# Kernel optimization log

Measured on AMD Instinct MI355X. Metric: run time of the kernel, lower is better.

Reference implementation:

```python
import jax, jax.numpy as jnp
import numpy as np

N, E = 50000, 800000
NFEAT, NHID, HEADS, NCLASS = 256, 16, 8, 40


def _gat_conv(x, src, dst, W, att_src, att_dst, bias, heads, out_ch, concat, num_nodes):
    # x: [N, F_in]; W: [F_in, heads*out_ch]; att_*: [heads, out_ch]; bias matches output dim
    h = (x @ W).reshape(num_nodes, heads, out_ch)          # [N, H, C]
    a_src = jnp.einsum('nhc,hc->nh', h, att_src)           # [N, H]
    a_dst = jnp.einsum('nhc,hc->nh', h, att_dst)           # [N, H]
    logits = jax.nn.leaky_relu(a_src[src] + a_dst[dst], negative_slope=0.2)  # [E, H]
    # segment softmax over incoming edges of each destination node
    m = jax.ops.segment_max(logits, dst, num_segments=num_nodes)
    e = jnp.exp(logits - m[dst])
    denom = jax.ops.segment_sum(e, dst, num_segments=num_nodes)
    alpha = e / (denom[dst] + 1e-16)                       # [E, H]
    msg = h[src] * alpha[:, :, None]                       # [E, H, C]
    out = jax.ops.segment_sum(msg, dst, num_segments=num_nodes)  # [N, H, C]
    out = out.reshape(num_nodes, heads * out_ch) if concat else out.mean(axis=1)
    return out + bias


def setup_inputs() -> dict:
    key = jax.random.key(0)
    ks = jax.random.split(key, 10)
    x = jax.random.normal(ks[0], (N, NFEAT), dtype=jnp.float32)
    edge_index = jax.random.randint(ks[1], (2, E), 0, N, dtype=jnp.int64)
    s = 0.1
    W1 = jax.random.normal(ks[2], (NFEAT, HEADS * NHID), dtype=jnp.float32) * s
    att_src1 = jax.random.normal(ks[3], (HEADS, NHID), dtype=jnp.float32) * s
    att_dst1 = jax.random.normal(ks[4], (HEADS, NHID), dtype=jnp.float32) * s
    b1 = jnp.zeros((HEADS * NHID,), dtype=jnp.float32)
    W2 = jax.random.normal(ks[5], (HEADS * NHID, NCLASS), dtype=jnp.float32) * s
    att_src2 = jax.random.normal(ks[6], (1, NCLASS), dtype=jnp.float32) * s
    att_dst2 = jax.random.normal(ks[7], (1, NCLASS), dtype=jnp.float32) * s
    b2 = jnp.zeros((NCLASS,), dtype=jnp.float32)
    return dict(x=x, edge_index=edge_index, W1=W1, att_src1=att_src1, att_dst1=att_dst1,
                b1=b1, W2=W2, att_src2=att_src2, att_dst2=att_dst2, b2=b2)


def reference(x, edge_index, W1, att_src1, att_dst1, b1, W2, att_src2, att_dst2, b2):
    # add self-loops (PyG GATConv default)
    loops = jnp.arange(N, dtype=edge_index.dtype)
    src = jnp.concatenate([edge_index[0], loops])
    dst = jnp.concatenate([edge_index[1], loops])
    # dropout layers are identity in eval mode
    h = _gat_conv(x, src, dst, W1, att_src1, att_dst1, b1, HEADS, NHID, True, N)
    h = jax.nn.elu(h)
    out = _gat_conv(h, src, dst, W2, att_src2, att_dst2, b2, 1, NCLASS, False, N)
    return jax.nn.log_softmax(out, axis=1)
```

## Files before the change

kernel.cpp:

```cpp
#include <hip/hip_runtime.h>
#include <math.h>

#define NODES 50000
#define NEDGE 800000
#define ETOT  (NEDGE + NODES)
#define NF    256
#define F1    128
#define NHEAD 8
#define NHID  16
#define NC    40
#define ELLCAP 64
#define SG_BLOCKS 4103
#define SG_GEMMCUT 3910

typedef __attribute__((ext_vector_type(8))) short bf16x8;
typedef __attribute__((ext_vector_type(4))) float f32x4;
typedef __attribute__((ext_vector_type(2))) float f32x2;

__device__ __forceinline__ float bflo(unsigned u) { return __uint_as_float(u << 16); }
__device__ __forceinline__ float bfhi(unsigned u) { return __uint_as_float(u & 0xffff0000u); }
__device__ __forceinline__ unsigned short f2bf(float f) {
    unsigned u = __float_as_uint(f);
    unsigned r = u + 0x7fffu + ((u >> 16) & 1u);
    return (unsigned short)(r >> 16);
}
__device__ __forceinline__ unsigned pk2(float a, float b) {
    return (unsigned)f2bf(a) | ((unsigned)f2bf(b) << 16);
}

__global__ void detect_k(const unsigned* __restrict__ u, unsigned* __restrict__ flag) {
    int t = threadIdx.x;
    if (u[2 * t + 1] != 0u) atomicOr(flag, 1u);
}

__global__ void prepW12(const float* __restrict__ W1, const float* __restrict__ atts1,
                        const float* __restrict__ attd1,
                        const float* __restrict__ W2, const float* __restrict__ atts2,
                        const float* __restrict__ attd2,
                        unsigned short* __restrict__ W1t, unsigned short* __restrict__ W2e) {
    int b = blockIdx.x;
    int k = threadIdx.x;
    if (b < 144) {
        int n = b;
        float v;
        if (n < 128) {
            v = W1[(size_t)k * F1 + n];
        } else if (n < 136) {
            int h = n - 128; v = 0.f;
#pragma unroll
            for (int c = 0; c < 16; ++c) v += W1[(size_t)k * F1 + h * 16 + c] * atts1[h * 16 + c];
        } else {
            int h = n - 136; v = 0.f;
#pragma unroll
            for (int c = 0; c < 16; ++c) v += W1[(size_t)k * F1 + h * 16 + c] * attd1[h * 16 + c];
        }
        W1t[(size_t)n * NF + k] = f2bf(v);
    } else {
        int n = b - 144;
        if (k >= F1) return;
        float v = 0.f;
        if (n < NC) {
            v = W2[(size_t)k * NC + n];
        } else if (n == NC) {
#pragma unroll
            for (int c = 0; c < NC; ++c) v += W2[(size_t)k * NC + c] * atts2[c];
        } else if (n == NC + 1) {
#pragma unroll
            for (int c = 0; c < NC; ++c) v += W2[(size_t)k * NC + c] * attd2[c];
        }
        W2e[(size_t)n * F1 + k] = f2bf(v);
    }
}

__global__ __launch_bounds__(256) void scatter_gemm1(
        const unsigned* __restrict__ u, const unsigned* __restrict__ flag,
        int* __restrict__ fill, unsigned short* __restrict__ csr16,
        const float* __restrict__ x, const unsigned short* __restrict__ W1t,
        unsigned char* __restrict__ h1f8, float* __restrict__ as1,
        float* __restrict__ ad1) {
    __shared__ uint4 wlds[2304];
    int bid = blockIdx.x;
    int t = threadIdx.x;
    bool isGemm = (bid < SG_GEMMCUT) && ((bid % 5) == 4);
    if (!isGemm) {
        int si = bid - min(bid, SG_GEMMCUT) / 5;
        int e = si * 256 + t;
        if (e >= ETOT) return;
        int s, d;
        if (e < NEDGE) {
            if (*flag) { s = (int)u[e]; d = (int)u[NEDGE + e]; }
            else       { s = (int)u[2 * e]; d = (int)u[2 * NEDGE + 2 * e]; }
        } else s = d = e - NEDGE;
        int pos = atomicAdd(&fill[d], 1);
        if (pos < ELLCAP) csr16[((size_t)d << 6) + pos] = (unsigned short)s;
        return;
    }
    int gi = bid / 5;
    int wave = t >> 6, lane = t & 63;
    int mbase = gi * 64 + wave * 16;
    int rowc = min(mbase + (lane & 15), NODES - 1);
    int kg = lane >> 4;
    const float4* xr = (const float4*)(x + (size_t)rowc * NF + kg * 8);

    float4 xa[16];
#pragma unroll
    for (int ks = 0; ks < 8; ++ks) {
        xa[2 * ks]     = xr[ks * 8];
        xa[2 * ks + 1] = xr[ks * 8 + 1];
    }
    __builtin_amdgcn_sched_barrier(0);

    f32x4 acc[9];
#pragma unroll
    for (int f = 0; f < 9; ++f) acc[f] = (f32x4){0.f, 0.f, 0.f, 0.f};

    int r = lane & 15;
    int swz = r & 7;
    int rb = r * 16 + kg;

#pragma unroll
    for (int half = 0; half < 2; ++half) {
        if (half) __syncthreads();
#pragma unroll
        for (int it = 0; it < 9; ++it) {
            int i = it * 256 + t;
            wlds[i ^ ((i >> 4) & 7)] = ((const uint4*)W1t)[(i >> 4) * 32 + half * 16 + (i & 15)];
        }
        __syncthreads();
#pragma unroll
        for (int ks = 0; ks < 4; ++ks) {
            union { uint4 u4; bf16x8 v; } A;
            float4 a0 = xa[2 * (half * 4 + ks)], a1 = xa[2 * (half * 4 + ks) + 1];
            A.u4.x = pk2(a0.x, a0.y); A.u4.y = pk2(a0.z, a0.w);
            A.u4.z = pk2(a1.x, a1.y); A.u4.w = pk2(a1.z, a1.w);
#pragma unroll
            for (int f = 0; f < 9; ++f) {
                union { uint4 u4; bf16x8 v; } B;
                B.u4 = wlds[(f * 256 + rb + ks * 4) ^ swz];
                acc[f] = __builtin_amdgcn_mfma_f32_16x16x32_bf16(A.v, B.v, acc[f], 0, 0, 0);
            }
        }
    }

    int col = lane & 15;
    int rbase = mbase + (lane >> 4) * 4;
#pragma unroll
    for (int f = 0; f < 8; ++f) {
        int w = 0;
        w = __builtin_amdgcn_cvt_pk_fp8_f32(acc[f][0], acc[f][1], w, false);
        w = __builtin_amdgcn_cvt_pk_fp8_f32(acc[f][2], acc[f][3], w, true);
#pragma unroll
        for (int i = 0; i < 4; ++i) {
            int rr = rbase + i;
            if (rr < NODES)
                h1f8[(size_t)rr * F1 + f * 16 + col] = (unsigned char)((w >> (8 * i)) & 0xff);
        }
    }
#pragma unroll
    for (int i = 0; i < 4; ++i) {
        int rr = rbase + i;
        if (rr < NODES) {
            float v = acc[8][i];
            if (col < 8) as1[(size_t)rr * NHEAD + col] = v;
            else ad1[(size_t)rr * NHEAD + (col - 8)] = v;
        }
    }
}

#define PROC8F8(AV, HV)                                          \
    {                                                            \
        float l = (AV) + adv;                                    \
        l = l > 0.f ? l : 0.2f * l;                              \
        float p = __expf(l);                                     \
        den += p;                                                \
        f32x2 c0 = __builtin_amdgcn_cvt_pk_f32_fp8(HV.x, false); \
        f32x2 c1 = __builtin_amdgcn_cvt_pk_f32_fp8(HV.x, true);  \
        f32x2 c2 = __builtin_amdgcn_cvt_pk_f32_fp8(HV.y, false); \
        f32x2 c3 = __builtin_amdgcn_cvt_pk_f32_fp8(HV.y, true);  \
        acc[0] += p * c0.x; acc[1] += p * c0.y;                  \
        acc[2] += p * c1.x; acc[3] += p * c1.y;                  \
        acc[4] += p * c2.x; acc[5] += p * c2.y;                  \
        acc[6] += p * c3.x; acc[7] += p * c3.y;                  \
    }

#define PROC8(AV, HV)                                    \
    {                                                    \
        float l = (AV) + adv;                            \
        l = l > 0.f ? l : 0.2f * l;                      \
        float p = __expf(l);                             \
        den += p;                                        \
        acc[0] += p * bflo(HV.x); acc[1] += p * bfhi(HV.x); \
        acc[2] += p * bflo(HV.y); acc[3] += p * bfhi(HV.y); \
        acc[4] += p * bflo(HV.z); acc[5] += p * bfhi(HV.z); \
        acc[6] += p * bflo(HV.w); acc[7] += p * bfhi(HV.w); \
    }

__global__ __launch_bounds__(256) void msg1g2(const int* __restrict__ fill,
                                              const unsigned short* __restrict__ csr16,
                                              const float* __restrict__ as1,
                                              const float* __restrict__ ad1,
                                              const unsigned char* __restrict__ h1f8,
                                              const float* __restrict__ b1,
                                              const unsigned short* __restrict__ W2e,
                                              unsigned short* __restrict__ h2b,
                                              float* __restrict__ as2,
                                              float* __restrict__ ad2) {
    __shared__ uint4 w2s[768];
    __shared__ uint4 o1s[256];
    int t = threadIdx.x;
    int wid = t >> 6, lane = t & 63;
    int g = lane >> 4;
    int cl = lane & 15;
    int h = cl >> 1;

#pragma unroll
    for (int it = 0; it < 3; ++it) {
        int i = it * 256 + t;
        w2s[i ^ ((i >> 4) & 7)] = ((const uint4*)W2e)[i];
    }

    int d = blockIdx.x * 16 + wid * 4 + g;
    float adv = ad1[(size_t)d * NHEAD + h];
    int deg = fill[d];
    size_t eb = (size_t)d << 6;
    float den = 0.f;
    float acc[8];
#pragma unroll
    for (int k = 0; k < 8; ++k) acc[k] = 0.f;

    const char* as1c = (const char*)as1;
    unsigned hoff = (unsigned)(h << 2);
    unsigned coff = (unsigned)(cl << 3);

#define LD1(J, AV, HV)                                                \
    {                                                                 \
        int j_ = (J);                                                 \
        AV = -1e30f; HV = make_uint2(0u, 0u);                         \
        if (j_ < deg) {                                               \
            unsigned ss = (unsigned)csr16[eb + j_];                   \
            AV = *(const float*)(as1c + (ss << 5) + hoff);            \
            HV = *(const uint2*)(h1f8 + (ss << 7) + coff);            \
        }                                                             \
    }

    float av0, av1; uint2 hv0, hv1;
    LD1(0, av0, hv0);
    LD1(1, av1, hv1);
    for (int j = 0; j < deg; j += 2) {
        float ta, tb; uint2 ua, ub;
        LD1(j + 2, ta, ua);
        LD1(j + 3, tb, ub);
        PROC8F8(av0, hv0);
        PROC8F8(av1, hv1);
        av0 = ta; hv0 = ua; av1 = tb; hv1 = ub;
    }
#undef LD1

    float invd = 1.f / (den + 1e-16f);
    const float4* bp = (const float4*)(b1 + cl * 8);
    float4 ba = bp[0], bb = bp[1];
    float v[8];
    v[0] = acc[0] * invd + ba.x; v[1] = acc[1] * invd + ba.y;
    v[2] = acc[2] * invd + ba.z; v[3] = acc[3] * invd + ba.w;
    v[4] = acc[4] * invd + bb.x; v[5] = acc[5] * invd + bb.y;
    v[6] = acc[6] * invd + bb.z; v[7] = acc[7] * invd + bb.w;
#pragma unroll
    for (int k = 0; k < 8; ++k) {
        float ev = __expf(v[k]) - 1.f;
        v[k] = v[k] > 0.f ? v[k] : ev;
    }
    uint4 o;
    o.x = pk2(v[0], v[1]); o.y = pk2(v[2], v[3]);
    o.z = pk2(v[4], v[5]); o.w = pk2(v[6], v[7]);
    int orow = wid * 4 + g;
    o1s[(orow * 16 + cl) ^ (orow & 7)] = o;
    __syncthreads();

    if (wid < 3) {
        int r = lane & 15;
        int kg = lane >> 4;
        int swz = r & 7;
        f32x4 c2 = (f32x4){0.f, 0.f, 0.f, 0.f};
#pragma unroll
        for (int ks = 0; ks < 4; ++ks) {
            union { uint4 u; bf16x8 vv; } A, B;
            A.u = o1s[(r * 16 + kg + ks * 4) ^ swz];
            B.u = w2s[(wid * 256 + r * 16 + kg + ks * 4) ^ swz];
            c2 = __builtin_amdgcn_mfma_f32_16x16x32_bf16(A.vv, B.vv, c2, 0, 0, 0);
        }
        int col = lane & 15;
        int rbase = blockIdx.x * 16 + (lane >> 4) * 4;
        if (wid < 2) {
#pragma unroll
            for (int i = 0; i < 4; ++i)
                h2b[(size_t)(rbase + i) * NC + wid * 16 + col] = f2bf(c2[i]);
        } else {
            int c = 32 + col;
#pragma unroll
            for (int i = 0; i < 4; ++i) {
                int rr = rbase + i;
                if (c < NC) h2b[(size_t)rr * NC + c] = f2bf(c2[i]);
                else if (c == NC) as2[rr] = c2[i];
                else if (c == NC + 1) ad2[rr] = c2[i];
            }
        }
    }
}

__global__ __launch_bounds__(256) void msg2(const int* __restrict__ fill,
                                            const unsigned short* __restrict__ csr16,
                                            const float* __restrict__ as2,
                                            const float* __restrict__ ad2,
                                            const unsigned short* __restrict__ h2b,
                                            const float* __restrict__ b2,
                                            float* __restrict__ out) {
    int t = threadIdx.x;
    int wid = t >> 6, lane = t & 63;
    int g = lane >> 3;
    int cl = lane & 7;
    int clc = cl < 5 ? cl : 4;
    bool act = cl < 5;
    int d0 = blockIdx.x * 32 + wid * 8 + g;
    int d = min(d0, NODES - 1);
    float adv = ad2[d];
    int deg = act ? fill[d] : 0;
    size_t eb = (size_t)d << 6;
    float den = 0.f;
    float acc[8];
#pragma unroll
    for (int k = 0; k < 8; ++k) acc[k] = 0.f;

    const char* as2c = (const char*)as2;
    const char* h2c = (const char*)h2b;
    unsigned coff = (unsigned)(clc << 4);

#define LD2(J, AV, HV)                                                \
    {                                                                 \
        int j_ = (J);                                                 \
        AV = -1e30f; HV = make_uint4(0u, 0u, 0u, 0u);                 \
        if (j_ < deg) {                                               \
            unsigned ss = (unsigned)csr16[eb + j_];                   \
            AV = *(const float*)(as2c + (ss << 2));                   \
            HV = *(const uint4*)(h2c + ss * 80u + coff);              \
        }                                                             \
    }

    float av0, av1; uint4 hv0, hv1;
    LD2(0, av0, hv0);
    LD2(1, av1, hv1);
    for (int j = 0; j < deg; j += 2) {
        float ta, tb; uint4 ua, ub;
        LD2(j + 2, ta, ua);
        LD2(j + 3, tb, ub);
        PROC8(av0, hv0);
        PROC8(av1, hv1);
        av0 = ta; hv0 = ua; av1 = tb; hv1 = ub;
    }
#undef LD2

    float invd = 1.f / (den + 1e-16f);
    float v[8];
    float mk = -1e30f;
    if (act) {
        const float4* bp = (const float4*)(b2 + cl * 8);
        float4 ba = bp[0], bb = bp[1];
        v[0] = acc[0] * invd + ba.x; v[1] = acc[1] * invd + ba.y;
        v[2] = acc[2] * invd + ba.z; v[3] = acc[3] * invd + ba.w;
        v[4] = acc[4] * invd + bb.x; v[5] = acc[5] * invd + bb.y;
        v[6] = acc[6] * invd + bb.z; v[7] = acc[7] * invd + bb.w;
#pragma unroll
        for (int k = 0; k < 8; ++k) mk = fmaxf(mk, v[k]);
    }
    mk = fmaxf(mk, __shfl_xor(mk, 1, 64));
    mk = fmaxf(mk, __shfl_xor(mk, 2, 64));
    mk = fmaxf(mk, __shfl_xor(mk, 4, 64));
    float e = 0.f;
    if (act) {
#pragma unroll
        for (int k = 0; k < 8; ++k) e += __expf(v[k] - mk);
    }
    e += __shfl_xor(e, 1, 64);
    e += __shfl_xor(e, 2, 64);
    e += __shfl_xor(e, 4, 64);
    float lse = mk + logf(e);
    if (act && d0 < NODES) {
        float4 o0 = make_float4(v[0] - lse, v[1] - lse, v[2] - lse, v[3] - lse);
        float4 o1 = make_float4(v[4] - lse, v[5] - lse, v[6] - lse, v[7] - lse);
        float* po = out + (size_t)d0 * NC + cl * 8;
        *(float4*)po = o0;
        *(float4*)(po + 4) = o1;
    }
}

extern "C" void kernel_launch(void* const* d_in, const int* in_sizes, int n_in,
                              void* d_out, int out_size, void* d_ws, size_t ws_size,
                              hipStream_t stream) {
    const float* x       = (const float*)d_in[0];
    const unsigned* eidx = (const unsigned*)d_in[1];
    const float* W1      = (const float*)d_in[2];
    const float* atts1   = (const float*)d_in[3];
    const float* attd1   = (const float*)d_in[4];
    const float* b1      = (const float*)d_in[5];
    const float* W2      = (const float*)d_in[6];
    const float* atts2   = (const float*)d_in[7];
    const float* attd2   = (const float*)d_in[8];
    const float* b2      = (const float*)d_in[9];
    float* out = (float*)d_out;

    char* base = (char*)d_ws;
    size_t off = 0;
    auto takeB = [&](size_t bytes) {
        void* p = base + off;
        off = (off + bytes + 255) & ~(size_t)255;
        return p;
    };
    unsigned* flag = (unsigned*)takeB(256);
    int* fill      = (int*)takeB((size_t)NODES * 4);
    unsigned short* csr16 = (unsigned short*)takeB((size_t)NODES * ELLCAP * 2 + 256);
    unsigned short* W1t  = (unsigned short*)takeB((size_t)144 * NF * 2);
    unsigned short* W2e  = (unsigned short*)takeB((size_t)48 * F1 * 2);
    unsigned char* h1f8  = (unsigned char*)takeB((size_t)NODES * F1);
    float* as1     = (float*)takeB((size_t)NODES * NHEAD * 4);
    float* ad1     = (float*)takeB((size_t)NODES * NHEAD * 4);
    unsigned short* h2b  = (unsigned short*)takeB((size_t)NODES * NC * 2 + 256);
    float* as2     = (float*)takeB((size_t)NODES * 4);
    float* ad2     = (float*)takeB((size_t)NODES * 4);

    hipMemsetAsync(flag, 0, 4, stream);
    hipMemsetAsync(fill, 0, (size_t)NODES * 4, stream);

    detect_k<<<1, 256, 0, stream>>>(eidx, flag);

    prepW12<<<192, 256, 0, stream>>>(W1, atts1, attd1, W2, atts2, attd2, W1t, W2e);

    scatter_gemm1<<<SG_BLOCKS, 256, 0, stream>>>(eidx, flag, fill, csr16,
                                                 x, W1t, h1f8, as1, ad1);

    msg1g2<<<NODES / 16, 256, 0, stream>>>(fill, csr16, as1, ad1, h1f8, b1,
                                           W2e, h2b, as2, ad2);

    msg2<<<(NODES + 31) / 32, 256, 0, stream>>>(fill, csr16, as2, ad2, h2b, b2, out);
}
```

Before: 124.7 us.

## Partition edge scatter by destination residue to keep atomics XCD-local

The edge scatter now gives each block a 2048-edge chunk. Eight blocks share each chunk, and each one handles only the destinations whose low three bits match its block-id residue. The intent is that blocks on the same XCD, given round-robin dispatch, touch only their own slice of the fill counters and ELL rows, so atomics and stores stay in that XCD's L2 instead of bouncing between caches. In exchange, every destination index is read eight times and the GEMM blocks are interleaved at a new ratio of 8 per 40-block window.

```diff
diff --git a/kernel.cpp b/kernel.cpp
--- a/kernel.cpp
+++ b/kernel.cpp
@@ -10,8 +10,10 @@
 #define NHID  16
 #define NC    40
 #define ELLCAP 64
-#define SG_BLOCKS 4103
-#define SG_GEMMCUT 3910
+#define SG_CHUNK 2048
+#define SG_NWIN 104
+#define SG_BLOCKS (SG_NWIN * 40)
+#define SG_GEMM 782
 
 typedef __attribute__((ext_vector_type(8))) short bf16x8;
 typedef __attribute__((ext_vector_type(4))) float f32x4;
@@ -81,21 +83,34 @@
     __shared__ uint4 wlds[2304];
     int bid = blockIdx.x;
     int t = threadIdx.x;
-    bool isGemm = (bid < SG_GEMMCUT) && ((bid % 5) == 4);
-    if (!isGemm) {
-        int si = bid - min(bid, SG_GEMMCUT) / 5;
-        int e = si * 256 + t;
-        if (e >= ETOT) return;
-        int s, d;
-        if (e < NEDGE) {
-            if (*flag) { s = (int)u[e]; d = (int)u[NEDGE + e]; }
-            else       { s = (int)u[2 * e]; d = (int)u[2 * NEDGE + 2 * e]; }
-        } else s = d = e - NEDGE;
-        int pos = atomicAdd(&fill[d], 1);
-        if (pos < ELLCAP) csr16[((size_t)d << 6) + pos] = (unsigned short)s;
+    int w = bid / 40, i = bid % 40;
+    if (i < 32) {
+        int chunk = w * 4 + (i >> 3);
+        int residue = bid & 7;
+        int ebase = chunk * SG_CHUNK;
+        bool isi32 = (*flag) != 0;
+#pragma unroll
+        for (int q = 0; q < 8; ++q) {
+            int e = ebase + q * 256 + t;
+            if (e < ETOT) {
+                int s, d;
+                if (e < NEDGE) {
+                    d = isi32 ? (int)u[NEDGE + e] : (int)u[2 * NEDGE + 2 * e];
+                } else {
+                    d = e - NEDGE;
+                }
+                if ((d & 7) == residue) {
+                    if (e < NEDGE) s = isi32 ? (int)u[e] : (int)u[2 * e];
+                    else s = d;
+                    int pos = atomicAdd(&fill[d], 1);
+                    if (pos < ELLCAP) csr16[((size_t)d << 6) + pos] = (unsigned short)s;
+                }
+            }
+        }
         return;
     }
-    int gi = bid / 5;
+    int gi = w * 8 + (i - 32);
+    if (gi >= SG_GEMM) return;
     int wave = t >> 6, lane = t & 63;
     int mbase = gi * 64 + wave * 16;
     int rowc = min(mbase + (lane & 15), NODES - 1);
@@ -123,8 +138,9 @@
         if (half) __syncthreads();
 #pragma unroll
         for (int it = 0; it < 9; ++it) {
-            int i = it * 256 + t;
-            wlds[i ^ ((i >> 4) & 7)] = ((const uint4*)W1t)[(i >> 4) * 32 + half * 16 + (i & 15)];
+            int idx = it * 256 + t;
+            wlds[idx ^ ((idx >> 4) & 7)] =
+                ((const uint4*)W1t)[(idx >> 4) * 32 + half * 16 + (idx & 15)];
         }
         __syncthreads();
 #pragma unroll
@@ -146,21 +162,21 @@
     int rbase = mbase + (lane >> 4) * 4;
 #pragma unroll
     for (int f = 0; f < 8; ++f) {
-        int w = 0;
-        w = __builtin_amdgcn_cvt_pk_fp8_f32(acc[f][0], acc[f][1], w, false);
-        w = __builtin_amdgcn_cvt_pk_fp8_f32(acc[f][2], acc[f][3], w, true);
-#pragma unroll
-        for (int i = 0; i < 4; ++i) {
-            int rr = rbase + i;
+        int wv = 0;
+        wv = __builtin_amdgcn_cvt_pk_fp8_f32(acc[f][0], acc[f][1], wv, false);
+        wv = __builtin_amdgcn_cvt_pk_fp8_f32(acc[f][2], acc[f][3], wv, true);
+#pragma unroll
+        for (int ii = 0; ii < 4; ++ii) {
+            int rr = rbase + ii;
             if (rr < NODES)
-                h1f8[(size_t)rr * F1 + f * 16 + col] = (unsigned char)((w >> (8 * i)) & 0xff);
-        }
-    }
-#pragma unroll
-    for (int i = 0; i < 4; ++i) {
-        int rr = rbase + i;
+                h1f8[(size_t)rr * F1 + f * 16 + col] = (unsigned char)((wv >> (8 * ii)) & 0xff);
+        }
+    }
+#pragma unroll
+    for (int ii = 0; ii < 4; ++ii) {
+        int rr = rbase + ii;
         if (rr < NODES) {
-            float v = acc[8][i];
+            float v = acc[8][ii];
             if (col < 8) as1[(size_t)rr * NHEAD + col] = v;
             else ad1[(size_t)rr * NHEAD + (col - 8)] = v;
         }
```

New measurement: 124.5 us. Within noise of the previous version (-0.1%).
